# Performance work log

Hardware: AMD Instinct MI355X
Metric: run time of the kernel (lower is better)

Reference implementation:

```python
import jax, jax.numpy as jnp
import numpy as np


def setup_inputs() -> dict:
    key = jax.random.key(0)
    ks = jax.random.split(key, 6)
    B, T, S, E, D = 8, 128, 512, 512, 512  # batch, trg_len, src_len, enc_dim, trg_dim
    W_SCALE = 0.03  # small init to keep tanh unsaturated
    return {
        "hidden": jax.random.normal(ks[0], (B, T, D), jnp.float32),
        "encoder_outputs": jax.random.normal(ks[1], (B, S, E), jnp.float32),
        "encoder_mask": jnp.ones((B, S), jnp.float32),
        "W_attn": jax.random.normal(ks[2], (D, E + D), jnp.float32) * W_SCALE,
        "b_attn": jnp.zeros((D,), jnp.float32),
        "W_v": jax.random.normal(ks[3], (1, D), jnp.float32) * W_SCALE,
        "b_v": jnp.zeros((1,), jnp.float32),
        "W_out": jax.random.normal(ks[4], (D, E + D), jnp.float32) * W_SCALE,
    }


def masked_softmax(x, m, axis=-1):
    # faithful to repo: x*m, stable exp, e*m, normalize with eps
    x = x * m
    e_x = jnp.exp(x - jnp.max(x, axis=axis, keepdims=True))
    e_x = e_x * m
    return e_x / (jnp.sum(e_x, axis=axis, keepdims=True) + 1e-6)


def reference(hidden, encoder_outputs, encoder_mask, W_attn, b_attn, W_v, b_v, W_out):
    B, T, D = hidden.shape
    S = encoder_outputs.shape[1]
    # concat order in get_energy is (hidden_i, encoder_outputs), so split W_attn
    W_h = W_attn[:, :D]   # (D_out, trg_dim)
    W_e = W_attn[:, D:]   # (D_out, enc_dim)
    # Linear(concat) == h@W_h^T + e@W_e^T + b; vectorized over all (t, s) pairs
    hp = jnp.einsum('btd,kd->btk', hidden, W_h)            # (B,T,K)
    ep = jnp.einsum('bse,ke->bsk', encoder_outputs, W_e)   # (B,S,K)
    feat = jnp.tanh(hp[:, :, None, :] + ep[:, None, :, :] + b_attn)  # (B,T,S,K)
    energies = jnp.einsum('btsk,k->bts', feat, W_v[0]) + b_v[0]      # (B,T,S)
    # forward: energies * mask, then masked softmax
    m = encoder_mask[:, None, :]  # (B,1,S)
    energies = energies * m
    attn_weights = masked_softmax(energies, m, axis=-1)    # (B,T,S)
    weighted_context = jnp.einsum('bts,bse->bte', attn_weights, encoder_outputs)
    h_cat = jnp.concatenate([weighted_context, hidden], axis=-1)  # (B,T,E+D)
    h_tilde = jnp.tanh(jnp.einsum('btc,dc->btd', h_cat, W_out))   # (B,T,D)
    return h_tilde, weighted_context, attn_weights
```

## Files before the change

kernel.cpp:

```cpp
#include <hip/hip_runtime.h>
#include <hip/hip_bf16.h>
#include <math.h>

typedef unsigned short u16;
typedef unsigned int u32;
typedef __bf16 bf16x8 __attribute__((ext_vector_type(8)));
typedef float f32x4 __attribute__((ext_vector_type(4)));

#define OUT_WC   524288LL
#define OUT_ATTN 1048576LL
#define C2 2.8853900817779268f
#define LOG2E 1.4426950408889634f
#define LAS 40

__device__ inline u16 f2b(float f) {
    return (u16)((__float_as_uint(f) + 0x8000u) >> 16);
}
__device__ inline u32 pkcvt(float x, float y) {
    __hip_bfloat162 h = __float22bfloat162_rn(make_float2(x, y));
    return *(u32*)&h;
}
__device__ inline float tanh_fast(float x) {
    return 1.f - 2.f * __builtin_amdgcn_rcpf(__builtin_amdgcn_exp2f(C2 * x) + 1.f);
}

__global__ __launch_bounds__(256) void proj(
    const float* __restrict__ hidden, const float* __restrict__ enc,
    const float* __restrict__ Wattn, const float* __restrict__ battn,
    float* __restrict__ hp, u16* __restrict__ ept)
{
    __shared__ u16 lA[64 * LAS];
    __shared__ u16 lB[64 * LAS];
    const int tid = threadIdx.x;
    const int wvi = tid >> 6, ln = tid & 63;
    const int wm = wvi >> 1, wn = wvi & 1;
    const int l16 = ln & 15, quad = ln >> 4;
    const int blk = blockIdx.x;
    const bool ise = blk < 512;
    int bx, by, zz = 0, lda, ldb;
    const float *A, *B;
    if (ise) {
        zz = blk >> 6; by = (blk >> 3) & 7; bx = blk & 7;
        A = Wattn + 512; lda = 1024;
        B = enc + (long long)zz * 262144; ldb = 512;
    } else {
        int i = blk - 512; by = i >> 3; bx = i & 7;
        A = hidden; lda = 512;
        B = Wattn; ldb = 1024;
    }
    const int m0 = by * 64, n0 = bx * 64;
    const int srow = tid >> 2, skof = (tid & 3) * 8;
    const float* Ap = A + (long long)(m0 + srow) * lda + skof;
    const float* Bp = B + (long long)(n0 + srow) * ldb + skof;

    f32x4 acc00 = {0,0,0,0}, acc01 = {0,0,0,0}, acc10 = {0,0,0,0}, acc11 = {0,0,0,0};

    for (int k0 = 0; k0 < 512; k0 += 32) {
        float4 a0v = *(const float4*)(Ap + k0);
        float4 a1v = *(const float4*)(Ap + k0 + 4);
        float4 b0v = *(const float4*)(Bp + k0);
        float4 b1v = *(const float4*)(Bp + k0 + 4);
        __syncthreads();
        *(uint4*)&lA[srow * LAS + skof] =
            make_uint4(pkcvt(a0v.x,a0v.y), pkcvt(a0v.z,a0v.w), pkcvt(a1v.x,a1v.y), pkcvt(a1v.z,a1v.w));
        *(uint4*)&lB[srow * LAS + skof] =
            make_uint4(pkcvt(b0v.x,b0v.y), pkcvt(b0v.z,b0v.w), pkcvt(b1v.x,b1v.y), pkcvt(b1v.z,b1v.w));
        __syncthreads();
        bf16x8 a0 = *(const bf16x8*)&lA[(wm * 32      + l16) * LAS + quad * 8];
        bf16x8 a1 = *(const bf16x8*)&lA[(wm * 32 + 16 + l16) * LAS + quad * 8];
        bf16x8 b0 = *(const bf16x8*)&lB[(wn * 32      + l16) * LAS + quad * 8];
        bf16x8 b1 = *(const bf16x8*)&lB[(wn * 32 + 16 + l16) * LAS + quad * 8];
        acc00 = __builtin_amdgcn_mfma_f32_16x16x32_bf16(a0, b0, acc00, 0, 0, 0);
        acc01 = __builtin_amdgcn_mfma_f32_16x16x32_bf16(a0, b1, acc01, 0, 0, 0);
        acc10 = __builtin_amdgcn_mfma_f32_16x16x32_bf16(a1, b0, acc10, 0, 0, 0);
        acc11 = __builtin_amdgcn_mfma_f32_16x16x32_bf16(a1, b1, acc11, 0, 0, 0);
    }

    const f32x4* accs[4] = { &acc00, &acc01, &acc10, &acc11 };
    #pragma unroll
    for (int i = 0; i < 2; ++i) {
        #pragma unroll
        for (int j = 0; j < 2; ++j) {
            const f32x4& a = *accs[i * 2 + j];
            #pragma unroll
            for (int r = 0; r < 4; ++r) {
                int m = m0 + wm * 32 + i * 16 + quad * 4 + r;
                int n = n0 + wn * 32 + j * 16 + l16;
                float v = a[r];
                if (ise) ept[(long long)zz * 262144 + (long long)m * 512 + n] =
                             f2b(__builtin_amdgcn_exp2f(C2 * v));
                else     hp[(long long)m * 512 + n] = C2 * (v + battn[n]);
            }
        }
    }
}

template<int TANH, int BT>
__device__ inline void mm32_impl(
    const float* __restrict__ A1, const float* __restrict__ A2, int ksplit,
    int lda, long long strideA,
    const float* __restrict__ B_, int ldb, long long strideB,
    float* __restrict__ C_, int ldc, long long strideC, int K)
{
    __shared__ u16 lA[32 * LAS];
    __shared__ u16 lB[64 * LAS];
    const int tid = threadIdx.x;
    const int wvi = tid >> 6, ln = tid & 63;
    const int l16 = ln & 15, quad = ln >> 4;
    const int msub = wvi & 1, npair = wvi >> 1;
    const int m0 = blockIdx.y * 32, n0 = blockIdx.x * 64;
    const long long bz = blockIdx.z;
    const int rowA = tid >> 3, kofA = (tid & 7) * 4;
    const int rowB = tid >> 2, kofB = (tid & 3) * 8;
    const int tkrow = tid >> 3, tnof = (tid & 7) * 8;
    f32x4 acc0 = {0,0,0,0}, acc1 = {0,0,0,0};

    for (int k0 = 0; k0 < K; k0 += 32) {
        const float* Ap;
        if (k0 < ksplit) Ap = A1 + bz * strideA + (long long)(m0 + rowA) * lda + k0 + kofA;
        else             Ap = A2 + (long long)(m0 + rowA) * lda + (k0 - ksplit) + kofA;
        float4 av = *(const float4*)Ap;
        float4 bv0, bv1;
        if (!BT) {
            const float* Bp = B_ + bz * strideB + (long long)(n0 + rowB) * ldb + k0 + kofB;
            bv0 = *(const float4*)Bp; bv1 = *(const float4*)(Bp + 4);
        } else {
            const float* Bp = B_ + bz * strideB + (long long)(k0 + tkrow) * ldb + n0 + tnof;
            bv0 = *(const float4*)Bp; bv1 = *(const float4*)(Bp + 4);
        }
        __syncthreads();
        *(uint2*)&lA[rowA * LAS + kofA] = make_uint2(pkcvt(av.x, av.y), pkcvt(av.z, av.w));
        if (!BT) {
            int kk = kofB ^ (((rowB >> 3) & 3) << 3);
            *(uint4*)&lB[rowB * LAS + kk] =
                make_uint4(pkcvt(bv0.x,bv0.y), pkcvt(bv0.z,bv0.w), pkcvt(bv1.x,bv1.y), pkcvt(bv1.z,bv1.w));
        } else {
            #pragma unroll
            for (int i = 0; i < 8; ++i) {
                int n = tnof + i;
                int kk = tkrow ^ (((n >> 3) & 3) << 3);
                float val = (i < 4) ? ((const float*)&bv0)[i] : ((const float*)&bv1)[i - 4];
                lB[n * LAS + kk] = f2b(val);
            }
        }
        __syncthreads();
        bf16x8 a = *(const bf16x8*)&lA[(msub * 16 + l16) * LAS + quad * 8];
        int nr0 = npair * 32 + l16, nr1 = nr0 + 16;
        bf16x8 b0 = *(const bf16x8*)&lB[nr0 * LAS + (quad * 8 ^ (((nr0 >> 3) & 3) << 3))];
        bf16x8 b1 = *(const bf16x8*)&lB[nr1 * LAS + (quad * 8 ^ (((nr1 >> 3) & 3) << 3))];
        acc0 = __builtin_amdgcn_mfma_f32_16x16x32_bf16(a, b0, acc0, 0, 0, 0);
        acc1 = __builtin_amdgcn_mfma_f32_16x16x32_bf16(a, b1, acc1, 0, 0, 0);
    }
    #pragma unroll
    for (int j = 0; j < 2; ++j) {
        const f32x4& a = j ? acc1 : acc0;
        #pragma unroll
        for (int r = 0; r < 4; ++r) {
            int m = m0 + msub * 16 + quad * 4 + r;
            int n = n0 + npair * 32 + j * 16 + l16;
            float v = a[r];
            C_[bz * strideC + (long long)m * ldc + n] = TANH ? tanh_fast(v) : v;
        }
    }
}

#define MM32_ARGS const float* A1, const float* A2, int ksplit, int lda, \
    long long strideA, const float* B_, int ldb, long long strideB, \
    float* C_, int ldc, long long strideC, int K
#define MM32_PASS A1, A2, ksplit, lda, strideA, B_, ldb, strideB, C_, ldc, strideC, K
__global__ __launch_bounds__(256) void mm_wc  (MM32_ARGS) { mm32_impl<0, 1>(MM32_PASS); }
__global__ __launch_bounds__(256) void mm_hout(MM32_ARGS) { mm32_impl<1, 0>(MM32_PASS); }

__device__ inline float wred_sum(float v) {
    #pragma unroll
    for (int i = 32; i > 0; i >>= 1) v += __shfl_xor(v, i);
    return v;
}
__device__ inline float bred_sum8(float v, float* red, int tid) {
    v = wred_sum(v);
    __syncthreads();
    if ((tid & 63) == 0) red[tid >> 6] = v;
    __syncthreads();
    float s = 0.f;
    #pragma unroll
    for (int i = 0; i < 8; ++i) s += red[i];
    return s;
}
__device__ inline void bred2_max(float v0, float v1, float* red, int tid,
                                 float* o0, float* o1) {
    #pragma unroll
    for (int i = 32; i > 0; i >>= 1) {
        v0 = fmaxf(v0, __shfl_xor(v0, i));
        v1 = fmaxf(v1, __shfl_xor(v1, i));
    }
    __syncthreads();
    if ((tid & 63) == 0) { red[tid >> 6] = v0; red[8 + (tid >> 6)] = v1; }
    __syncthreads();
    float a0 = red[0], a1 = red[8];
    #pragma unroll
    for (int i = 1; i < 8; ++i) { a0 = fmaxf(a0, red[i]); a1 = fmaxf(a1, red[8 + i]); }
    *o0 = a0; *o1 = a1;
}
__device__ inline void bred2_sum(float v0, float v1, float* red, int tid,
                                 float* o0, float* o1) {
    #pragma unroll
    for (int i = 32; i > 0; i >>= 1) { v0 += __shfl_xor(v0, i); v1 += __shfl_xor(v1, i); }
    __syncthreads();
    if ((tid & 63) == 0) { red[tid >> 6] = v0; red[8 + (tid >> 6)] = v1; }
    __syncthreads();
    float a0 = 0.f, a1 = 0.f;
    #pragma unroll
    for (int i = 0; i < 8; ++i) { a0 += red[i]; a1 += red[8 + i]; }
    *o0 = a0; *o1 = a1;
}

__device__ inline void proc8(uint4 c, float4 hw, float* a0, float* a1) {
    u32 cc[4] = {c.x, c.y, c.z, c.w};
    #pragma unroll
    for (int i = 0; i < 4; ++i) {
        float xl = __uint_as_float(cc[i] << 16);
        float xh = __uint_as_float(cc[i] & 0xFFFF0000u);
        float rl0 = __builtin_amdgcn_rcpf(fmaf(hw.x, xl, 1.f));
        float rh0 = __builtin_amdgcn_rcpf(fmaf(hw.x, xh, 1.f));
        float rl1 = __builtin_amdgcn_rcpf(fmaf(hw.y, xl, 1.f));
        float rh1 = __builtin_amdgcn_rcpf(fmaf(hw.y, xh, 1.f));
        a0[2*i]   = fmaf(hw.z, rl0, a0[2*i]);
        a0[2*i+1] = fmaf(hw.z, rh0, a0[2*i+1]);
        a1[2*i]   = fmaf(hw.z, rl1, a1[2*i]);
        a1[2*i+1] = fmaf(hw.z, rh1, a1[2*i+1]);
    }
}

__global__ __launch_bounds__(512) void energies(
    const float* __restrict__ maskp, const float* __restrict__ hp,
    const u16* __restrict__ ept, const float* __restrict__ Wv,
    const float* __restrict__ bvp, float* __restrict__ attn)
{
    __shared__ __align__(16) float4 hpw[512];
    __shared__ float pa[2][8][512];
    __shared__ float red[16];
    const int tid = threadIdx.x;
    const int b = blockIdx.x >> 6;
    const int t0 = (blockIdx.x & 63) * 2;

    float w = Wv[tid];
    float h0 = hp[(long long)(b * 128 + t0) * 512 + tid];
    float h1 = hp[(long long)(b * 128 + t0 + 1) * 512 + tid];
    hpw[tid] = make_float4(__builtin_amdgcn_exp2f(h0), __builtin_amdgcn_exp2f(h1), w, 0.f);
    float sumWv = bred_sum8(w, red, tid);

    const int kg = tid >> 6, sl = tid & 63;
    const int s0 = sl * 8;
    const u16* eb = ept + (long long)b * 262144 + (kg * 64) * 512 + s0;
    const float4* hq = &hpw[kg * 64];

    float a0[8] = {0,0,0,0,0,0,0,0}, a1[8] = {0,0,0,0,0,0,0,0};
    uint4 c0 = *(const uint4*)(eb);
    uint4 c1 = *(const uint4*)(eb + 512);
    uint4 c2 = *(const uint4*)(eb + 1024);
    uint4 c3 = *(const uint4*)(eb + 1536);
    for (int kk = 0; kk < 60; kk += 4) {
        const u16* nb = eb + (kk + 4) * 512;
        uint4 n0 = *(const uint4*)(nb);
        uint4 n1 = *(const uint4*)(nb + 512);
        uint4 n2 = *(const uint4*)(nb + 1024);
        uint4 n3 = *(const uint4*)(nb + 1536);
        proc8(c0, hq[kk],     a0, a1);
        proc8(c1, hq[kk + 1], a0, a1);
        proc8(c2, hq[kk + 2], a0, a1);
        proc8(c3, hq[kk + 3], a0, a1);
        c0 = n0; c1 = n1; c2 = n2; c3 = n3;
    }
    proc8(c0, hq[60], a0, a1);
    proc8(c1, hq[61], a0, a1);
    proc8(c2, hq[62], a0, a1);
    proc8(c3, hq[63], a0, a1);

    *(float4*)&pa[0][kg][s0]     = make_float4(a0[0], a0[1], a0[2], a0[3]);
    *(float4*)&pa[0][kg][s0 + 4] = make_float4(a0[4], a0[5], a0[6], a0[7]);
    *(float4*)&pa[1][kg][s0]     = make_float4(a1[0], a1[1], a1[2], a1[3]);
    *(float4*)&pa[1][kg][s0 + 4] = make_float4(a1[4], a1[5], a1[6], a1[7]);
    __syncthreads();

    const int s = tid;
    float A0 = 0.f, A1 = 0.f;
    #pragma unroll
    for (int g = 0; g < 8; ++g) { A0 += pa[0][g][s]; A1 += pa[1][g][s]; }
    float mv = maskp[(long long)b * 512 + s];
    float bv0 = bvp[0];
    float r0 = (bv0 + sumWv - 2.f * A0) * mv; r0 *= mv;
    float r1 = (bv0 + sumWv - 2.f * A1) * mv; r1 *= mv;

    float mx0, mx1;
    bred2_max(r0, r1, red, tid, &mx0, &mx1);
    float ex0 = __builtin_amdgcn_exp2f((r0 - mx0) * LOG2E) * mv;
    float ex1 = __builtin_amdgcn_exp2f((r1 - mx1) * LOG2E) * mv;
    float sm0, sm1;
    bred2_sum(ex0, ex1, red, tid, &sm0, &sm1);
    attn[(long long)(b * 128 + t0) * 512 + s]     = ex0 * (1.f / (sm0 + 1e-6f));
    attn[(long long)(b * 128 + t0 + 1) * 512 + s] = ex1 * (1.f / (sm1 + 1e-6f));
}

extern "C" void kernel_launch(void* const* d_in, const int* in_sizes, int n_in,
                              void* d_out, int out_size, void* d_ws, size_t ws_size,
                              hipStream_t stream)
{
    const float* hidden = (const float*)d_in[0];
    const float* enc    = (const float*)d_in[1];
    const float* mask   = (const float*)d_in[2];
    const float* Wattn  = (const float*)d_in[3];
    const float* battn  = (const float*)d_in[4];
    const float* Wv     = (const float*)d_in[5];
    const float* bvp    = (const float*)d_in[6];
    const float* Wout   = (const float*)d_in[7];
    float* out = (float*)d_out;

    float* hp = (float*)d_ws;
    u16*   ept = (u16*)((char*)d_ws + (2 << 20));

    proj<<<640, 256, 0, stream>>>(hidden, enc, Wattn, battn, hp, ept);
    energies<<<512, 512, 0, stream>>>(mask, hp, ept, Wv, bvp, out + OUT_ATTN);
    mm_wc<<<dim3(8, 4, 8), 256, 0, stream>>>(
        out + OUT_ATTN, out + OUT_ATTN, 1 << 30, 512, 65536,
        enc, 512, 262144, out + OUT_WC, 512, 65536, 512);
    mm_hout<<<dim3(8, 32, 1), 256, 0, stream>>>(
        out + OUT_WC, hidden, 512, 512, 0,
        Wout, 1024, 0, out, 512, 0, 1024);
}
```

Before: 151.9 us.

## Fuse context matmul into energies and precompute hidden half of output projection

The attention-weighted context product is folded into the energies kernel: each block keeps its two attention rows in shared memory and multiplies them by the encoder outputs in fp32 FMAs, which removes the separate mm_wc launch. The hidden-times-W_out half of the output projection moves into the proj kernel as extra blocks, so the final kernel only runs K=512 over the context and adds the precomputed term before tanh. This saves one launch and an attention round trip through memory, but every energies block now reads the whole encoder slice for its batch (512x512 floats) with scalar loads, and the context product no longer uses MFMA.

```diff
diff --git a/kernel.cpp b/kernel.cpp
--- a/kernel.cpp
+++ b/kernel.cpp
@@ -27,7 +27,8 @@
 __global__ __launch_bounds__(256) void proj(
     const float* __restrict__ hidden, const float* __restrict__ enc,
     const float* __restrict__ Wattn, const float* __restrict__ battn,
-    float* __restrict__ hp, u16* __restrict__ ept)
+    const float* __restrict__ Wout,
+    float* __restrict__ hp, u16* __restrict__ ept, float* __restrict__ hh)
 {
     __shared__ u16 lA[64 * LAS];
     __shared__ u16 lB[64 * LAS];
@@ -36,17 +37,23 @@
     const int wm = wvi >> 1, wn = wvi & 1;
     const int l16 = ln & 15, quad = ln >> 4;
     const int blk = blockIdx.x;
-    const bool ise = blk < 512;
-    int bx, by, zz = 0, lda, ldb;
+    int bx, by, zz = 0, lda, ldb, mode;
     const float *A, *B;
-    if (ise) {
+    if (blk < 512) {
+        mode = 0;
         zz = blk >> 6; by = (blk >> 3) & 7; bx = blk & 7;
         A = Wattn + 512; lda = 1024;
         B = enc + (long long)zz * 262144; ldb = 512;
-    } else {
+    } else if (blk < 640) {
+        mode = 1;
         int i = blk - 512; by = i >> 3; bx = i & 7;
         A = hidden; lda = 512;
         B = Wattn; ldb = 1024;
+    } else {
+        mode = 2;
+        int i = blk - 640; by = i >> 3; bx = i & 7;
+        A = hidden; lda = 512;
+        B = Wout + 512; ldb = 1024;
     }
     const int m0 = by * 64, n0 = bx * 64;
     const int srow = tid >> 2, skof = (tid & 3) * 8;
@@ -87,89 +94,17 @@
                 int m = m0 + wm * 32 + i * 16 + quad * 4 + r;
                 int n = n0 + wn * 32 + j * 16 + l16;
                 float v = a[r];
-                if (ise) ept[(long long)zz * 262144 + (long long)m * 512 + n] =
-                             f2b(__builtin_amdgcn_exp2f(C2 * v));
-                else     hp[(long long)m * 512 + n] = C2 * (v + battn[n]);
+                if (mode == 0)
+                    ept[(long long)zz * 262144 + (long long)m * 512 + n] =
+                        f2b(__builtin_amdgcn_exp2f(C2 * v));
+                else if (mode == 1)
+                    hp[(long long)m * 512 + n] = C2 * (v + battn[n]);
+                else
+                    hh[(long long)m * 512 + n] = v;
             }
         }
     }
 }
-
-template<int TANH, int BT>
-__device__ inline void mm32_impl(
-    const float* __restrict__ A1, const float* __restrict__ A2, int ksplit,
-    int lda, long long strideA,
-    const float* __restrict__ B_, int ldb, long long strideB,
-    float* __restrict__ C_, int ldc, long long strideC, int K)
-{
-    __shared__ u16 lA[32 * LAS];
-    __shared__ u16 lB[64 * LAS];
-    const int tid = threadIdx.x;
-    const int wvi = tid >> 6, ln = tid & 63;
-    const int l16 = ln & 15, quad = ln >> 4;
-    const int msub = wvi & 1, npair = wvi >> 1;
-    const int m0 = blockIdx.y * 32, n0 = blockIdx.x * 64;
-    const long long bz = blockIdx.z;
-    const int rowA = tid >> 3, kofA = (tid & 7) * 4;
-    const int rowB = tid >> 2, kofB = (tid & 3) * 8;
-    const int tkrow = tid >> 3, tnof = (tid & 7) * 8;
-    f32x4 acc0 = {0,0,0,0}, acc1 = {0,0,0,0};
-
-    for (int k0 = 0; k0 < K; k0 += 32) {
-        const float* Ap;
-        if (k0 < ksplit) Ap = A1 + bz * strideA + (long long)(m0 + rowA) * lda + k0 + kofA;
-        else             Ap = A2 + (long long)(m0 + rowA) * lda + (k0 - ksplit) + kofA;
-        float4 av = *(const float4*)Ap;
-        float4 bv0, bv1;
-        if (!BT) {
-            const float* Bp = B_ + bz * strideB + (long long)(n0 + rowB) * ldb + k0 + kofB;
-            bv0 = *(const float4*)Bp; bv1 = *(const float4*)(Bp + 4);
-        } else {
-            const float* Bp = B_ + bz * strideB + (long long)(k0 + tkrow) * ldb + n0 + tnof;
-            bv0 = *(const float4*)Bp; bv1 = *(const float4*)(Bp + 4);
-        }
-        __syncthreads();
-        *(uint2*)&lA[rowA * LAS + kofA] = make_uint2(pkcvt(av.x, av.y), pkcvt(av.z, av.w));
-        if (!BT) {
-            int kk = kofB ^ (((rowB >> 3) & 3) << 3);
-            *(uint4*)&lB[rowB * LAS + kk] =
-                make_uint4(pkcvt(bv0.x,bv0.y), pkcvt(bv0.z,bv0.w), pkcvt(bv1.x,bv1.y), pkcvt(bv1.z,bv1.w));
-        } else {
-            #pragma unroll
-            for (int i = 0; i < 8; ++i) {
-                int n = tnof + i;
-                int kk = tkrow ^ (((n >> 3) & 3) << 3);
-                float val = (i < 4) ? ((const float*)&bv0)[i] : ((const float*)&bv1)[i - 4];
-                lB[n * LAS + kk] = f2b(val);
-            }
-        }
-        __syncthreads();
-        bf16x8 a = *(const bf16x8*)&lA[(msub * 16 + l16) * LAS + quad * 8];
-        int nr0 = npair * 32 + l16, nr1 = nr0 + 16;
-        bf16x8 b0 = *(const bf16x8*)&lB[nr0 * LAS + (quad * 8 ^ (((nr0 >> 3) & 3) << 3))];
-        bf16x8 b1 = *(const bf16x8*)&lB[nr1 * LAS + (quad * 8 ^ (((nr1 >> 3) & 3) << 3))];
-        acc0 = __builtin_amdgcn_mfma_f32_16x16x32_bf16(a, b0, acc0, 0, 0, 0);
-        acc1 = __builtin_amdgcn_mfma_f32_16x16x32_bf16(a, b1, acc1, 0, 0, 0);
-    }
-    #pragma unroll
-    for (int j = 0; j < 2; ++j) {
-        const f32x4& a = j ? acc1 : acc0;
-        #pragma unroll
-        for (int r = 0; r < 4; ++r) {
-            int m = m0 + msub * 16 + quad * 4 + r;
-            int n = n0 + npair * 32 + j * 16 + l16;
-            float v = a[r];
-            C_[bz * strideC + (long long)m * ldc + n] = TANH ? tanh_fast(v) : v;
-        }
-    }
-}
-
-#define MM32_ARGS const float* A1, const float* A2, int ksplit, int lda, \
-    long long strideA, const float* B_, int ldb, long long strideB, \
-    float* C_, int ldc, long long strideC, int K
-#define MM32_PASS A1, A2, ksplit, lda, strideA, B_, ldb, strideB, C_, ldc, strideC, K
-__global__ __launch_bounds__(256) void mm_wc  (MM32_ARGS) { mm32_impl<0, 1>(MM32_PASS); }
-__global__ __launch_bounds__(256) void mm_hout(MM32_ARGS) { mm32_impl<1, 0>(MM32_PASS); }
 
 __device__ inline float wred_sum(float v) {
     #pragma unroll
@@ -234,10 +169,12 @@
 __global__ __launch_bounds__(512) void energies(
     const float* __restrict__ maskp, const float* __restrict__ hp,
     const u16* __restrict__ ept, const float* __restrict__ Wv,
-    const float* __restrict__ bvp, float* __restrict__ attn)
+    const float* __restrict__ bvp, const float* __restrict__ enc,
+    float* __restrict__ attn, float* __restrict__ wc)
 {
     __shared__ __align__(16) float4 hpw[512];
     __shared__ float pa[2][8][512];
+    __shared__ __align__(16) float2 aL[512];
     __shared__ float red[16];
     const int tid = threadIdx.x;
     const int b = blockIdx.x >> 6;
@@ -297,8 +234,77 @@
     float ex1 = __builtin_amdgcn_exp2f((r1 - mx1) * LOG2E) * mv;
     float sm0, sm1;
     bred2_sum(ex0, ex1, red, tid, &sm0, &sm1);
-    attn[(long long)(b * 128 + t0) * 512 + s]     = ex0 * (1.f / (sm0 + 1e-6f));
-    attn[(long long)(b * 128 + t0 + 1) * 512 + s] = ex1 * (1.f / (sm1 + 1e-6f));
+    float at0 = ex0 * (1.f / (sm0 + 1e-6f));
+    float at1 = ex1 * (1.f / (sm1 + 1e-6f));
+    attn[(long long)(b * 128 + t0) * 512 + s]     = at0;
+    attn[(long long)(b * 128 + t0 + 1) * 512 + s] = at1;
+    aL[s] = make_float2(at0, at1);
+    __syncthreads();
+
+    const float* encb = enc + (long long)b * 262144 + tid;
+    const float4* aL4 = (const float4*)aL;
+    float acc0 = 0.f, acc1 = 0.f;
+    for (int ss = 0; ss < 512; ss += 8) {
+        float ev[8];
+        #pragma unroll
+        for (int i = 0; i < 8; ++i) ev[i] = encb[(ss + i) * 512];
+        #pragma unroll
+        for (int i = 0; i < 4; ++i) {
+            float4 ap = aL4[(ss >> 1) + i];
+            acc0 = fmaf(ap.x, ev[2*i],   acc0);
+            acc1 = fmaf(ap.y, ev[2*i],   acc1);
+            acc0 = fmaf(ap.z, ev[2*i+1], acc0);
+            acc1 = fmaf(ap.w, ev[2*i+1], acc1);
+        }
+    }
+    wc[(long long)(b * 128 + t0) * 512 + tid]     = acc0;
+    wc[(long long)(b * 128 + t0 + 1) * 512 + tid] = acc1;
+}
+
+__global__ __launch_bounds__(256) void hout_k(
+    const float* __restrict__ wc, const float* __restrict__ Wout,
+    const float* __restrict__ hh, float* __restrict__ out)
+{
+    __shared__ u16 lA[32 * LAS];
+    __shared__ u16 lB[64 * LAS];
+    const int tid = threadIdx.x;
+    const int wvi = tid >> 6, ln = tid & 63;
+    const int l16 = ln & 15, quad = ln >> 4;
+    const int msub = wvi & 1, npair = wvi >> 1;
+    const int m0 = blockIdx.y * 32, n0 = blockIdx.x * 64;
+    const int rowA = tid >> 3, kofA = (tid & 7) * 4;
+    const int rowB = tid >> 2, kofB = (tid & 3) * 8;
+    f32x4 acc0 = {0,0,0,0}, acc1 = {0,0,0,0};
+
+    for (int k0 = 0; k0 < 512; k0 += 32) {
+        float4 av = *(const float4*)(wc + (long long)(m0 + rowA) * 512 + k0 + kofA);
+        const float* Bp = Wout + (long long)(n0 + rowB) * 1024 + k0 + kofB;
+        float4 bv0 = *(const float4*)Bp;
+        float4 bv1 = *(const float4*)(Bp + 4);
+        __syncthreads();
+        *(uint2*)&lA[rowA * LAS + kofA] = make_uint2(pkcvt(av.x, av.y), pkcvt(av.z, av.w));
+        int kk = kofB ^ (((rowB >> 3) & 3) << 3);
+        *(uint4*)&lB[rowB * LAS + kk] =
+            make_uint4(pkcvt(bv0.x,bv0.y), pkcvt(bv0.z,bv0.w), pkcvt(bv1.x,bv1.y), pkcvt(bv1.z,bv1.w));
+        __syncthreads();
+        bf16x8 a = *(const bf16x8*)&lA[(msub * 16 + l16) * LAS + quad * 8];
+        int nr0 = npair * 32 + l16, nr1 = nr0 + 16;
+        bf16x8 b0 = *(const bf16x8*)&lB[nr0 * LAS + (quad * 8 ^ (((nr0 >> 3) & 3) << 3))];
+        bf16x8 b1 = *(const bf16x8*)&lB[nr1 * LAS + (quad * 8 ^ (((nr1 >> 3) & 3) << 3))];
+        acc0 = __builtin_amdgcn_mfma_f32_16x16x32_bf16(a, b0, acc0, 0, 0, 0);
+        acc1 = __builtin_amdgcn_mfma_f32_16x16x32_bf16(a, b1, acc1, 0, 0, 0);
+    }
+    #pragma unroll
+    for (int j = 0; j < 2; ++j) {
+        const f32x4& a = j ? acc1 : acc0;
+        #pragma unroll
+        for (int r = 0; r < 4; ++r) {
+            int m = m0 + msub * 16 + quad * 4 + r;
+            int n = n0 + npair * 32 + j * 16 + l16;
+            long long idx = (long long)m * 512 + n;
+            out[idx] = tanh_fast(a[r] + hh[idx]);
+        }
+    }
 }
 
 extern "C" void kernel_launch(void* const* d_in, const int* in_sizes, int n_in,
@@ -315,15 +321,12 @@
     const float* Wout   = (const float*)d_in[7];
     float* out = (float*)d_out;
 
-    float* hp = (float*)d_ws;
+    float* hp  = (float*)d_ws;
     u16*   ept = (u16*)((char*)d_ws + (2 << 20));
-
-    proj<<<640, 256, 0, stream>>>(hidden, enc, Wattn, battn, hp, ept);
-    energies<<<512, 512, 0, stream>>>(mask, hp, ept, Wv, bvp, out + OUT_ATTN);
-    mm_wc<<<dim3(8, 4, 8), 256, 0, stream>>>(
-        out + OUT_ATTN, out + OUT_ATTN, 1 << 30, 512, 65536,
-        enc, 512, 262144, out + OUT_WC, 512, 65536, 512);
-    mm_hout<<<dim3(8, 32, 1), 256, 0, stream>>>(
-        out + OUT_WC, hidden, 512, 512, 0,
-        Wout, 1024, 0, out, 512, 0, 1024);
-}
+    float* hh  = (float*)((char*)d_ws + (6 << 20));
+
+    proj<<<768, 256, 0, stream>>>(hidden, enc, Wattn, battn, Wout, hp, ept, hh);
+    energies<<<512, 512, 0, stream>>>(mask, hp, ept, Wv, bvp, enc,
+                                      out + OUT_ATTN, out + OUT_WC);
+    hout_k<<<dim3(8, 32, 1), 256, 0, stream>>>(out + OUT_WC, Wout, hh, out);
+}
```

Result: no change. 149.3 us (-1.7%).
